# Kernel optimization log

Measured on AMD Instinct MI355X. Metric: run time of the kernel, lower is better.

Reference implementation:

```python
import jax, jax.numpy as jnp
import numpy as np

D_IN, D_OUT, N_TOK = 4096, 4096, 8192

def _binarize(w):
    # sign with straight-through estimator (sign(0) treated as sign output of jnp.sign)
    return w + jax.lax.stop_gradient(jnp.sign(w) - w)

def setup_inputs() -> dict:
    key = jax.random.key(0)
    k1, k2, k3, k4, k5 = jax.random.split(key, 5)
    x = jax.random.normal(k1, (N_TOK, D_IN), dtype=jnp.float32)
    W1 = jax.random.normal(k2, (D_OUT, D_IN), dtype=jnp.float32)
    W2 = jax.random.normal(k3, (D_OUT, D_IN), dtype=jnp.float32)
    b1 = jax.random.normal(k4, (D_OUT,), dtype=jnp.float32)
    b2 = jax.random.normal(k5, (D_OUT,), dtype=jnp.float32)
    return {"x": x, "W1": W1, "W2": W2, "b1": b1, "b2": b2}

def reference(x, W1, W2, b1, b2):
    # BinaryLinear: F.linear(x, sign(W), b); TernaryLinear = binary1(x) - binary2(x)
    out1 = x @ _binarize(W1).T + b1
    out2 = x @ _binarize(W2).T + b2
    return out1 - out2
```

## Files before the change

### kernel.cpp

```cpp
#include <hip/hip_runtime.h>


#define DIM_K 4096
#define DIM_N 4096
#define DIM_M 8192

typedef _Float16 f16x8 __attribute__((ext_vector_type(8)));
typedef _Float16 f16x4 __attribute__((ext_vector_type(4)));
typedef float    f32x4 __attribute__((ext_vector_type(4)));


__global__ void cvt_x_kernel(const float4* __restrict__ x, f16x4* __restrict__ xh) {
    const int i = blockIdx.x * blockDim.x + threadIdx.x;
    const float4 v = x[i];
    f16x4 h;
    h[0] = (_Float16)v.x; h[1] = (_Float16)v.y;
    h[2] = (_Float16)v.z; h[3] = (_Float16)v.w;
    xh[i] = h;
}

__device__ __forceinline__ float signdiff(float a, float b) {
    const float sa = (float)((a > 0.f) - (a < 0.f));
    const float sb = (float)((b > 0.f) - (b < 0.f));
    return sa - sb;
}

__global__ void cvt_w_kernel(const float4* __restrict__ w1,
                             const float4* __restrict__ w2,
                             f16x4* __restrict__ wh) {
    const int i = blockIdx.x * blockDim.x + threadIdx.x;
    const float4 a = w1[i];
    const float4 b = w2[i];
    f16x4 h;
    h[0] = (_Float16)signdiff(a.x, b.x);
    h[1] = (_Float16)signdiff(a.y, b.y);
    h[2] = (_Float16)signdiff(a.z, b.z);
    h[3] = (_Float16)signdiff(a.w, b.w);
    wh[i] = h;
}

__global__ void cvt_b_kernel(const float* __restrict__ b1,
                             const float* __restrict__ b2,
                             float* __restrict__ bd) {
    const int i = blockIdx.x * blockDim.x + threadIdx.x;
    bd[i] = b1[i] - b2[i];
}


__global__ __launch_bounds__(256, 2) void ternary_gemm(
    const _Float16* __restrict__ Xh, const _Float16* __restrict__ Wh,
    const float* __restrict__ bd, float* __restrict__ C) {
    __shared__ __align__(16) char smem[32768];

    const int tid  = threadIdx.x;
    const int wave = tid >> 6;
    const int lane = tid & 63;
    const int wm = wave >> 1, wn = wave & 1;
    const int q = lane >> 4, r = lane & 15;

    const int lrow   = lane >> 3;
    const int lchunk = lane & 7;
    const int gchunk = lchunk ^ lrow;
    const int srow   = wave * 8 + lrow;

    const int bRowM = blockIdx.y * 128;
    const int bColN = blockIdx.x * 128;

    const char* aPtr = (const char*)Xh + (size_t)(bRowM + srow) * (DIM_K * 2) + gchunk * 16;
    const char* bPtr = (const char*)Wh + (size_t)(bColN + srow) * (DIM_K * 2) + gchunk * 16;

    char* const ldsA = smem + wave * 1024;
    char* const ldsB = smem + 16384 + wave * 1024;

    const char* const aRd = smem + (wm * 64 + r) * 128;
    const char* const bRd = smem + 16384 + (wn * 64 + r) * 128;
    const int sc0 = ((0 * 4 + q) ^ (r & 7)) * 16;
    const int sc1 = ((1 * 4 + q) ^ (r & 7)) * 16;

    f32x4 acc[4][4] = {};

    for (int kt = 0; kt < DIM_K; kt += 64) {
        __syncthreads();
#pragma unroll
        for (int i = 0; i < 4; ++i) {
            __builtin_amdgcn_global_load_lds(
                (const __attribute__((address_space(1))) void*)(aPtr + (size_t)i * 262144),
                (__attribute__((address_space(3))) void*)(ldsA + i * 4096), 16, 0, 0);
            __builtin_amdgcn_global_load_lds(
                (const __attribute__((address_space(1))) void*)(bPtr + (size_t)i * 262144),
                (__attribute__((address_space(3))) void*)(ldsB + i * 4096), 16, 0, 0);
        }
        __syncthreads();

#pragma unroll
        for (int kk = 0; kk < 2; ++kk) {
            const int sc = kk ? sc1 : sc0;
            f16x8 af[4], bf[4];
#pragma unroll
            for (int t = 0; t < 4; ++t) {
                af[t] = *(const f16x8*)(aRd + t * 2048 + sc);
                bf[t] = *(const f16x8*)(bRd + t * 2048 + sc);
            }
#pragma unroll
            for (int im = 0; im < 4; ++im)
#pragma unroll
                for (int in = 0; in < 4; ++in)
                    acc[im][in] = __builtin_amdgcn_mfma_f32_16x16x32_f16(
                        af[im], bf[in], acc[im][in], 0, 0, 0);
        }
        aPtr += 128;
        bPtr += 128;
    }

    const int col0 = bColN + wn * 64 + r;
    const int row0 = bRowM + wm * 64 + q * 4;
    float bias[4];
#pragma unroll
    for (int in = 0; in < 4; ++in) bias[in] = bd[col0 + in * 16];
#pragma unroll
    for (int im = 0; im < 4; ++im) {
#pragma unroll
        for (int in = 0; in < 4; ++in) {
            const f32x4 v = acc[im][in];
            const int col = col0 + in * 16;
            const size_t base = (size_t)(row0 + im * 16) * DIM_N + col;
#pragma unroll
            for (int j = 0; j < 4; ++j)
                C[base + (size_t)j * DIM_N] = v[j] + bias[in];
        }
    }
}


extern "C" void kernel_launch(void* const* d_in, const int* in_sizes, int n_in,
                              void* d_out, int out_size, void* d_ws, size_t ws_size,
                              hipStream_t stream) {
    const float* x  = (const float*)d_in[0];
    const float* W1 = (const float*)d_in[1];
    const float* W2 = (const float*)d_in[2];
    const float* b1 = (const float*)d_in[3];
    const float* b2 = (const float*)d_in[4];
    float* out = (float*)d_out;

    _Float16* Xh = (_Float16*)d_ws;
    _Float16* Wh = (_Float16*)((char*)d_ws + (size_t)67108864);
    float*    bd = (float*)((char*)d_ws + (size_t)67108864 + 33554432);
    (void)ws_size; (void)in_sizes; (void)n_in; (void)out_size;

    cvt_x_kernel<<<32768, 256, 0, stream>>>((const float4*)x, (f16x4*)Xh);
    cvt_w_kernel<<<16384, 256, 0, stream>>>((const float4*)W1, (const float4*)W2, (f16x4*)Wh);
    cvt_b_kernel<<<16, 256, 0, stream>>>(b1, b2, bd);

    ternary_gemm<<<dim3(32, 64), 256, 0, stream>>>(Xh, Wh, bd, out);
}
```

Measured before the change: 553.6 us.

## Register-prefetch next K tile to overlap global loads with MFMA compute

```diff
diff --git a/kernel.cpp b/kernel.cpp
--- a/kernel.cpp
+++ b/kernel.cpp
@@ -47,7 +47,7 @@
 }
 
 
-__global__ __launch_bounds__(256, 2) void ternary_gemm(
+__global__ __launch_bounds__(256, 3) void ternary_gemm(
     const _Float16* __restrict__ Xh, const _Float16* __restrict__ Wh,
     const float* __restrict__ bd, float* __restrict__ C) {
     __shared__ __align__(16) char smem[32768];
@@ -58,19 +58,18 @@
     const int wm = wave >> 1, wn = wave & 1;
     const int q = lane >> 4, r = lane & 15;
 
-    const int lrow   = lane >> 3;
-    const int lchunk = lane & 7;
-    const int gchunk = lchunk ^ lrow;
-    const int srow   = wave * 8 + lrow;
+    const int srow  = tid >> 3;
+    const int chunk = tid & 7;
+    const int swz   = ((chunk ^ (srow & 7)) << 4);
 
     const int bRowM = blockIdx.y * 128;
     const int bColN = blockIdx.x * 128;
 
-    const char* aPtr = (const char*)Xh + (size_t)(bRowM + srow) * (DIM_K * 2) + gchunk * 16;
-    const char* bPtr = (const char*)Wh + (size_t)(bColN + srow) * (DIM_K * 2) + gchunk * 16;
+    const char* aG = (const char*)Xh + (size_t)(bRowM + srow) * (DIM_K * 2) + (chunk << 4);
+    const char* bG = (const char*)Wh + (size_t)(bColN + srow) * (DIM_K * 2) + (chunk << 4);
 
-    char* const ldsA = smem + wave * 1024;
-    char* const ldsB = smem + 16384 + wave * 1024;
+    char* const aW = smem + srow * 128 + swz;
+    char* const bW = smem + 16384 + srow * 128 + swz;
 
     const char* const aRd = smem + (wm * 64 + r) * 128;
     const char* const bRd = smem + 16384 + (wn * 64 + r) * 128;
@@ -78,19 +77,28 @@
     const int sc1 = ((1 * 4 + q) ^ (r & 7)) * 16;
 
     f32x4 acc[4][4] = {};
+    int4 av[4], bv[4];
 
-    for (int kt = 0; kt < DIM_K; kt += 64) {
-        __syncthreads();
+#pragma unroll
+    for (int i = 0; i < 4; ++i) {
+        av[i] = *(const int4*)(aG + (size_t)i * 262144);
+        bv[i] = *(const int4*)(bG + (size_t)i * 262144);
+    }
+    aG += 128; bG += 128;
+#pragma unroll
+    for (int i = 0; i < 4; ++i) {
+        *(int4*)(aW + i * 4096) = av[i];
+        *(int4*)(bW + i * 4096) = bv[i];
+    }
+    __syncthreads();
+
+    for (int kt = 1; kt < 64; ++kt) {
 #pragma unroll
         for (int i = 0; i < 4; ++i) {
-            __builtin_amdgcn_global_load_lds(
-                (const __attribute__((address_space(1))) void*)(aPtr + (size_t)i * 262144),
-                (__attribute__((address_space(3))) void*)(ldsA + i * 4096), 16, 0, 0);
-            __builtin_amdgcn_global_load_lds(
-                (const __attribute__((address_space(1))) void*)(bPtr + (size_t)i * 262144),
-                (__attribute__((address_space(3))) void*)(ldsB + i * 4096), 16, 0, 0);
+            av[i] = *(const int4*)(aG + (size_t)i * 262144);
+            bv[i] = *(const int4*)(bG + (size_t)i * 262144);
         }
-        __syncthreads();
+        aG += 128; bG += 128;
 
 #pragma unroll
         for (int kk = 0; kk < 2; ++kk) {
@@ -108,8 +116,31 @@
                     acc[im][in] = __builtin_amdgcn_mfma_f32_16x16x32_f16(
                         af[im], bf[in], acc[im][in], 0, 0, 0);
         }
-        aPtr += 128;
-        bPtr += 128;
+
+        __syncthreads();
+#pragma unroll
+        for (int i = 0; i < 4; ++i) {
+            *(int4*)(aW + i * 4096) = av[i];
+            *(int4*)(bW + i * 4096) = bv[i];
+        }
+        __syncthreads();
+    }
+
+#pragma unroll
+    for (int kk = 0; kk < 2; ++kk) {
+        const int sc = kk ? sc1 : sc0;
+        f16x8 af[4], bf[4];
+#pragma unroll
+        for (int t = 0; t < 4; ++t) {
+            af[t] = *(const f16x8*)(aRd + t * 2048 + sc);
+            bf[t] = *(const f16x8*)(bRd + t * 2048 + sc);
+        }
+#pragma unroll
+        for (int im = 0; im < 4; ++im)
+#pragma unroll
+            for (int in = 0; in < 4; ++in)
+                acc[im][in] = __builtin_amdgcn_mfma_f32_16x16x32_f16(
+                    af[im], bf[in], acc[im][in], 0, 0, 0);
     }
 
     const int col0 = bColN + wn * 64 + r;
```

After: 2.061 ms. +272.3%, slower.
